# Optimization experiments

Hardware: AMD Instinct MI355X
Metric: run time of the kernel (lower is better)

The kernel has to match this reference:

```python
import jax, jax.numpy as jnp
import numpy as np

N = 16384
E = 524288
IN_DIM, H1, H2 = 256, 128, 64


def setup_inputs() -> dict:
    key = jax.random.key(0)
    ks = jax.random.split(key, 9)
    features = jax.random.normal(ks[0], (N, IN_DIM), dtype=jnp.float32)
    src = jax.random.randint(ks[1], (E,), 0, N, dtype=jnp.int32)
    dst = jax.random.randint(ks[2], (E,), 0, N, dtype=jnp.int32)
    s = 0.1
    W1 = jax.random.normal(ks[3], (IN_DIM, H1), dtype=jnp.float32) * s
    b1 = jnp.zeros((H1,), dtype=jnp.float32)
    W2 = jax.random.normal(ks[4], (H1, H1), dtype=jnp.float32) * s
    b2 = jnp.zeros((H1,), dtype=jnp.float32)
    W3 = jax.random.normal(ks[5], (H1, H2), dtype=jnp.float32) * s
    b3 = jnp.zeros((H2,), dtype=jnp.float32)
    return {"features": features, "src": src, "dst": dst,
            "W1": W1, "b1": b1, "W2": W2, "b2": b2, "W3": W3, "b3": b3}


def _degree_norms(src, dst):
    ones = jnp.ones(src.shape[0], dtype=jnp.float32)
    deg_out = jax.ops.segment_sum(ones, src, num_segments=N)
    deg_in = jax.ops.segment_sum(ones, dst, num_segments=N)
    # allow_zero_in_degree=True with norm='both': clamp degree to min 1
    norm_out = jax.lax.rsqrt(jnp.maximum(deg_out, 1.0))  # [N]
    norm_in = jax.lax.rsqrt(jnp.maximum(deg_in, 1.0))    # [N]
    return norm_out, norm_in


def _graph_conv(h, src, dst, norm_out, norm_in, W, b, relu):
    # DGL GraphConv, norm='both': D_in^{-1/2} A^T (D_out^{-1/2} h) W + b
    h = h * norm_out[:, None]
    msg = h[src]                                   # gather [E, d]
    agg = jax.ops.segment_sum(msg, dst, num_segments=N)  # scatter-add [N, d]
    out = agg * norm_in[:, None] @ W + b
    return jax.nn.relu(out) if relu else out


def reference(features, src, dst, W1, b1, W2, b2, W3, b3):
    norm_out, norm_in = _degree_norms(src, dst)
    h = _graph_conv(features, src, dst, norm_out, norm_in, W1, b1, True)
    h = _graph_conv(h, src, dst, norm_out, norm_in, W2, b2, True)
    z = _graph_conv(h, src, dst, norm_out, norm_in, W3, b3, False)  # [N, H2]
    adj_rec = jax.nn.sigmoid(z @ z.T)  # [N, N]
    return adj_rec, z
```

## Files before the change

### kernel.cpp

```cpp
#include <hip/hip_runtime.h>
#include <hip/hip_bf16.h>

#define NN 16384
#define EE 524288

constexpr int D0 = 256, D1 = 128, D2 = 64;

typedef __attribute__((ext_vector_type(8))) short short8;
typedef __attribute__((ext_vector_type(4))) float f32x4;

__device__ __forceinline__ float b2f(ushort u) {
  union { unsigned int i; float f; } x;
  x.i = ((unsigned int)u) << 16;
  return x.f;
}


__global__ __launch_bounds__(256) void count_deg_kernel(
    const int* __restrict__ src, const int* __restrict__ dst,
    int* __restrict__ deg_out, int* __restrict__ deg_in) {
  int e = blockIdx.x * 256 + threadIdx.x;
  if (e < EE) {
    atomicAdd(&deg_out[src[e]], 1);
    atomicAdd(&deg_in[dst[e]], 1);
  }
}

__global__ __launch_bounds__(256) void norm_kernel(
    const int* __restrict__ deg_out, const int* __restrict__ deg_in,
    float* __restrict__ norm_out, float* __restrict__ norm_in) {
  int i = blockIdx.x * 256 + threadIdx.x;
  if (i < NN) {
    norm_out[i] = rsqrtf(fmaxf((float)deg_out[i], 1.0f));
    norm_in[i]  = rsqrtf(fmaxf((float)deg_in[i], 1.0f));
  }
}

__global__ __launch_bounds__(256) void prefix_kernel(
    const int* __restrict__ deg_in, int* __restrict__ row_ptr,
    int* __restrict__ cursor) {
  __shared__ int part[256];
  int t = threadIdx.x;
  int base = t * 64;
  int s = 0;
  for (int j = 0; j < 64; ++j) s += deg_in[base + j];
  part[t] = s;
  __syncthreads();
  for (int off = 1; off < 256; off <<= 1) {
    int add = (t >= off) ? part[t - off] : 0;
    __syncthreads();
    part[t] += add;
    __syncthreads();
  }
  int run = (t == 0) ? 0 : part[t - 1];
  for (int j = 0; j < 64; ++j) {
    row_ptr[base + j] = run;
    cursor[base + j] = run;
    run += deg_in[base + j];
  }
  if (t == 255) row_ptr[NN] = run;
}

__global__ __launch_bounds__(256) void fill_csr_kernel(
    const int* __restrict__ src, const int* __restrict__ dst,
    int* __restrict__ cursor, int* __restrict__ csr_src) {
  int e = blockIdx.x * 256 + threadIdx.x;
  if (e < EE) {
    int pos = atomicAdd(&cursor[dst[e]], 1);
    csr_src[pos] = src[e];
  }
}


template<int DIN, int DOUT, bool OBF16>
__global__ __launch_bounds__(256) void gemm_kernel(
    const float* __restrict__ h, const float* __restrict__ W,
    const float* __restrict__ norm_out, float* __restrict__ tf,
    ushort* __restrict__ tb) {
  constexpr int W4 = DOUT / 4;
  constexpr int RG = 256 / W4;
  constexpr int RPT = 32 / RG;
  __shared__ float A[32][DIN];
  int tid = threadIdx.x;
  int r0 = blockIdx.x * 32;
  constexpr int NF4 = 32 * DIN / 4;
  for (int q = tid; q < NF4; q += 256) {
    int r = q / (DIN / 4);
    int c = q % (DIN / 4);
    float4 x = *(const float4*)&h[(size_t)(r0 + r) * DIN + c * 4];
    float no = norm_out[r0 + r];
    x.x *= no; x.y *= no; x.z *= no; x.w *= no;
    *(float4*)&A[r][c * 4] = x;
  }
  __syncthreads();
  int c4 = tid % W4;
  int rg = tid / W4;
  float4 acc[RPT];
#pragma unroll
  for (int j = 0; j < RPT; ++j) acc[j] = make_float4(0.f, 0.f, 0.f, 0.f);
  const float* Wp = W + c4 * 4;
#pragma unroll 2
  for (int k = 0; k < DIN; ++k) {
    float4 w = *(const float4*)&Wp[(size_t)k * DOUT];
#pragma unroll
    for (int j = 0; j < RPT; ++j) {
      float a = A[rg + j * RG][k];
      acc[j].x += a * w.x; acc[j].y += a * w.y;
      acc[j].z += a * w.z; acc[j].w += a * w.w;
    }
  }
#pragma unroll
  for (int j = 0; j < RPT; ++j) {
    size_t row = (size_t)(r0 + rg + j * RG);
    if (OBF16) {
      ushort4 o;
      __hip_bfloat16 h0 = __float2bfloat16(acc[j].x);
      __hip_bfloat16 h1 = __float2bfloat16(acc[j].y);
      __hip_bfloat16 h2 = __float2bfloat16(acc[j].z);
      __hip_bfloat16 h3 = __float2bfloat16(acc[j].w);
      o.x = *reinterpret_cast<ushort*>(&h0);
      o.y = *reinterpret_cast<ushort*>(&h1);
      o.z = *reinterpret_cast<ushort*>(&h2);
      o.w = *reinterpret_cast<ushort*>(&h3);
      *(ushort4*)&tb[row * DOUT + c4 * 4] = o;
    } else {
      *(float4*)&tf[row * DOUT + c4 * 4] = acc[j];
    }
  }
}


template<int DOUT, bool RELU>
__global__ __launch_bounds__(256) void gather_bf16_kernel(
    const ushort* __restrict__ t, const float* __restrict__ bias,
    const float* __restrict__ norm_in, const int* __restrict__ row_ptr,
    const int* __restrict__ csr, float* __restrict__ out) {
  constexpr int G8 = DOUT / 8;
  constexpr int S = 256 / G8;
  __shared__ float red[S][G8][8];
  int tid = threadIdx.x;
  int c8 = tid % G8, slot = tid / G8;
  int v = blockIdx.x;
  int k0 = row_ptr[v], k1 = row_ptr[v + 1];
  float a[8];
#pragma unroll
  for (int i = 0; i < 8; ++i) a[i] = 0.f;
  for (int k = k0 + slot; k < k1; k += S) {
    int s = csr[k];
    short8 m = *(const short8*)&t[(size_t)s * DOUT + c8 * 8];
#pragma unroll
    for (int i = 0; i < 8; ++i) a[i] += b2f((ushort)m[i]);
  }
#pragma unroll
  for (int i = 0; i < 8; ++i) red[slot][c8][i] = a[i];
  __syncthreads();
#pragma unroll
  for (int s = S / 2; s >= 1; s >>= 1) {
    if (slot < s) {
#pragma unroll
      for (int i = 0; i < 8; ++i) red[slot][c8][i] += red[slot + s][c8][i];
    }
    __syncthreads();
  }
  if (tid < G8) {
    float ni = norm_in[v];
    float o[8];
#pragma unroll
    for (int i = 0; i < 8; ++i) {
      o[i] = red[0][tid][i] * ni + bias[tid * 8 + i];
      if (RELU) o[i] = fmaxf(o[i], 0.f);
    }
    *(float4*)&out[(size_t)v * DOUT + tid * 8] = make_float4(o[0], o[1], o[2], o[3]);
    *(float4*)&out[(size_t)v * DOUT + tid * 8 + 4] = make_float4(o[4], o[5], o[6], o[7]);
  }
}


template<int DOUT, bool RELU>
__global__ __launch_bounds__(256) void gather_f32_kernel(
    const float* __restrict__ t, const float* __restrict__ bias,
    const float* __restrict__ norm_in, const int* __restrict__ row_ptr,
    const int* __restrict__ csr, float* __restrict__ out,
    ushort* __restrict__ zb) {
  constexpr int W4 = DOUT / 4;
  constexpr int S = 256 / W4;
  __shared__ float4 red[256];
  int tid = threadIdx.x;
  int c4 = tid % W4, slot = tid / W4;
  int v = blockIdx.x;
  int k0 = row_ptr[v], k1 = row_ptr[v + 1];
  float4 acc = make_float4(0.f, 0.f, 0.f, 0.f);
  for (int k = k0 + slot; k < k1; k += S) {
    int s = csr[k];
    float4 m = *(const float4*)&t[(size_t)s * DOUT + c4 * 4];
    acc.x += m.x; acc.y += m.y; acc.z += m.z; acc.w += m.w;
  }
  red[tid] = acc;
  __syncthreads();
  if (tid < W4) {
    float4 a = red[tid];
#pragma unroll
    for (int s = 1; s < S; ++s) {
      float4 b = red[s * W4 + tid];
      a.x += b.x; a.y += b.y; a.z += b.z; a.w += b.w;
    }
    float ni = norm_in[v];
    float4 b4 = *(const float4*)&bias[tid * 4];
    a.x = a.x * ni + b4.x; a.y = a.y * ni + b4.y;
    a.z = a.z * ni + b4.z; a.w = a.w * ni + b4.w;
    if (RELU) {
      a.x = fmaxf(a.x, 0.f); a.y = fmaxf(a.y, 0.f);
      a.z = fmaxf(a.z, 0.f); a.w = fmaxf(a.w, 0.f);
    }
    *(float4*)&out[(size_t)v * DOUT + tid * 4] = a;
    float vals[4] = {a.x, a.y, a.z, a.w};
    ushort4 ob;
    __hip_bfloat16 h0 = __float2bfloat16(vals[0]);
    __hip_bfloat16 h1 = __float2bfloat16(vals[1]);
    __hip_bfloat16 h2 = __float2bfloat16(vals[2]);
    __hip_bfloat16 h3 = __float2bfloat16(vals[3]);
    ob.x = *reinterpret_cast<ushort*>(&h0);
    ob.y = *reinterpret_cast<ushort*>(&h1);
    ob.z = *reinterpret_cast<ushort*>(&h2);
    ob.w = *reinterpret_cast<ushort*>(&h3);
    *(ushort4*)&zb[(size_t)v * DOUT + tid * 4] = ob;
  }
}


__global__ __launch_bounds__(256) void adj_mfma_kernel(
    const ushort* __restrict__ zb, float* __restrict__ C) {
  __shared__ ushort ZR[128 * 64];
  __shared__ ushort ZC[128 * 64];
  int t = threadIdx.x;
  int bx = blockIdx.x & 127, by = blockIdx.x >> 7;
  int row0 = by * 128, col0 = bx * 128;
  {
    int r = t >> 1;
    int ub = (t & 1) * 4;
    const float4* zr = (const float4*)(zb + (size_t)(row0 + r) * 64);
    const float4* zc = (const float4*)(zb + (size_t)(col0 + r) * 64);
    float4* LR = (float4*)ZR;
    float4* LC = (float4*)ZC;
#pragma unroll
    for (int u = 0; u < 4; ++u) {
      int sw = (ub + u) ^ (r & 7);
      LR[r * 8 + sw] = zr[ub + u];
      LC[r * 8 + sw] = zc[ub + u];
    }
  }
  __syncthreads();
  int l = t & 63, w = t >> 6;
  int wy = w >> 1, wx = w & 1;
  int lr = l & 15, lg = l >> 4;
  f32x4 acc[4][4];
#pragma unroll
  for (int i = 0; i < 4; ++i)
#pragma unroll
    for (int j = 0; j < 4; ++j) acc[i][j] = (f32x4){0.f, 0.f, 0.f, 0.f};

#pragma unroll
  for (int ks = 0; ks < 2; ++ks) {
    short8 af[4], bf_[4];
    int u = ks * 4 + lg;
#pragma unroll
    for (int i = 0; i < 4; ++i) {
      int ar = wy * 64 + i * 16 + lr;
      af[i] = *(const short8*)&ZR[ar * 64 + ((u ^ (ar & 7)) << 3)];
      int ac = wx * 64 + i * 16 + lr;
      bf_[i] = *(const short8*)&ZC[ac * 64 + ((u ^ (ac & 7)) << 3)];
    }
#pragma unroll
    for (int i = 0; i < 4; ++i)
#pragma unroll
      for (int j = 0; j < 4; ++j)
        acc[i][j] = __builtin_amdgcn_mfma_f32_16x16x32_bf16(
            bf_[j], af[i], acc[i][j], 0, 0, 0);
  }

#pragma unroll
  for (int i = 0; i < 4; ++i) {
    int crow = row0 + wy * 64 + i * 16 + lr;
    float* Crow = C + (size_t)crow * NN;
#pragma unroll
    for (int j = 0; j < 4; ++j) {
      int ccol = col0 + wx * 64 + j * 16 + lg * 4;
      float4 o;
      o.x = __builtin_amdgcn_rcpf(1.0f + __expf(-acc[i][j][0]));
      o.y = __builtin_amdgcn_rcpf(1.0f + __expf(-acc[i][j][1]));
      o.z = __builtin_amdgcn_rcpf(1.0f + __expf(-acc[i][j][2]));
      o.w = __builtin_amdgcn_rcpf(1.0f + __expf(-acc[i][j][3]));
      *(float4*)&Crow[ccol] = o;
    }
  }
}


extern "C" void kernel_launch(void* const* d_in, const int* in_sizes, int n_in,
                              void* d_out, int out_size, void* d_ws, size_t ws_size,
                              hipStream_t stream) {
  const float* features = (const float*)d_in[0];
  const int* src = (const int*)d_in[1];
  const int* dst = (const int*)d_in[2];
  const float* W1 = (const float*)d_in[3];
  const float* b1 = (const float*)d_in[4];
  const float* W2 = (const float*)d_in[5];
  const float* b2 = (const float*)d_in[6];
  const float* W3 = (const float*)d_in[7];
  const float* b3 = (const float*)d_in[8];

  float* outp = (float*)d_out;
  float* adj = outp;
  float* z = outp + (size_t)NN * NN;

  ushort* tb = (ushort*)adj;
  float* hbuf = adj + (size_t)NN * 64;
  float* t3 = adj + (size_t)NN * 192;

  float* wsf = (float*)d_ws;
  float* norm_out = wsf;
  float* norm_in = wsf + NN;
  int* deg_out = (int*)(wsf + 2 * NN);
  int* deg_in = deg_out + NN;
  int* row_ptr = deg_in + NN;
  int* cursor = row_ptr + NN + 256;
  int* csr_src = cursor + NN;
  ushort* zb = (ushort*)(csr_src + EE);

  hipMemsetAsync(deg_out, 0, 2 * NN * sizeof(int), stream);
  count_deg_kernel<<<EE / 256, 256, 0, stream>>>(src, dst, deg_out, deg_in);
  norm_kernel<<<NN / 256, 256, 0, stream>>>(deg_out, deg_in, norm_out, norm_in);
  prefix_kernel<<<1, 256, 0, stream>>>(deg_in, row_ptr, cursor);
  fill_csr_kernel<<<EE / 256, 256, 0, stream>>>(src, dst, cursor, csr_src);

  gemm_kernel<D0, D1, true><<<NN / 32, 256, 0, stream>>>(
      features, W1, norm_out, nullptr, tb);
  gather_bf16_kernel<D1, true><<<NN, 256, 0, stream>>>(
      tb, b1, norm_in, row_ptr, csr_src, hbuf);
  gemm_kernel<D1, D1, true><<<NN / 32, 256, 0, stream>>>(
      hbuf, W2, norm_out, nullptr, tb);
  gather_bf16_kernel<D1, true><<<NN, 256, 0, stream>>>(
      tb, b2, norm_in, row_ptr, csr_src, hbuf);
  gemm_kernel<D1, D2, false><<<NN / 32, 256, 0, stream>>>(
      hbuf, W3, norm_out, t3, nullptr);
  gather_f32_kernel<D2, false><<<NN, 256, 0, stream>>>(
      t3, b3, norm_in, row_ptr, csr_src, z, zb);

  adj_mfma_kernel<<<(NN / 128) * (NN / 128), 256, 0, stream>>>(zb, adj);
}
```

Before: 478.1 us.

## Use one wave per node for gathers, stage W in LDS, nontemporal adj stores

The aggregation kernels now assign one 64-lane wave per destination node, four nodes per block, and reduce across lanes with xor shuffles. This replaces the block-per-node layout whose LDS tree reduction and barriers left most threads idle at an average degree of about 32. The dense GEMM now stages W chunks in shared memory instead of reading them from global memory on every k step. The 1 GiB sigmoid adjacency output is written with nontemporal stores to avoid polluting the caches. These are several unrelated changes, and the extra LDS for W lowers the occupancy of the GEMM kernel.

```diff
diff --git a/kernel.cpp b/kernel.cpp
--- a/kernel.cpp
+++ b/kernel.cpp
@@ -13,6 +13,10 @@
   union { unsigned int i; float f; } x;
   x.i = ((unsigned int)u) << 16;
   return x.f;
+}
+__device__ __forceinline__ ushort f2b(float f) {
+  __hip_bfloat16 h = __float2bfloat16(f);
+  return *reinterpret_cast<ushort*>(&h);
 }
 
 
@@ -80,7 +84,9 @@
   constexpr int W4 = DOUT / 4;
   constexpr int RG = 256 / W4;
   constexpr int RPT = 32 / RG;
+  constexpr int KC = 64;
   __shared__ float A[32][DIN];
+  __shared__ float WC[KC][DOUT];
   int tid = threadIdx.x;
   int r0 = blockIdx.x * 32;
   constexpr int NF4 = 32 * DIN / 4;
@@ -92,21 +98,26 @@
     x.x *= no; x.y *= no; x.z *= no; x.w *= no;
     *(float4*)&A[r][c * 4] = x;
   }
-  __syncthreads();
   int c4 = tid % W4;
   int rg = tid / W4;
   float4 acc[RPT];
 #pragma unroll
   for (int j = 0; j < RPT; ++j) acc[j] = make_float4(0.f, 0.f, 0.f, 0.f);
-  const float* Wp = W + c4 * 4;
-#pragma unroll 2
-  for (int k = 0; k < DIN; ++k) {
-    float4 w = *(const float4*)&Wp[(size_t)k * DOUT];
-#pragma unroll
-    for (int j = 0; j < RPT; ++j) {
-      float a = A[rg + j * RG][k];
-      acc[j].x += a * w.x; acc[j].y += a * w.y;
-      acc[j].z += a * w.z; acc[j].w += a * w.w;
+
+  for (int kc = 0; kc < DIN / KC; ++kc) {
+    __syncthreads();
+    for (int q = tid; q < KC * W4; q += 256)
+      ((float4*)WC)[q] = ((const float4*)W)[(size_t)kc * KC * W4 + q];
+    __syncthreads();
+#pragma unroll 4
+    for (int k2 = 0; k2 < KC; ++k2) {
+      float4 w = *(const float4*)&WC[k2][c4 * 4];
+#pragma unroll
+      for (int j = 0; j < RPT; ++j) {
+        float a = A[rg + j * RG][kc * KC + k2];
+        acc[j].x += a * w.x; acc[j].y += a * w.y;
+        acc[j].z += a * w.z; acc[j].w += a * w.w;
+      }
     }
   }
 #pragma unroll
@@ -114,14 +125,8 @@
     size_t row = (size_t)(r0 + rg + j * RG);
     if (OBF16) {
       ushort4 o;
-      __hip_bfloat16 h0 = __float2bfloat16(acc[j].x);
-      __hip_bfloat16 h1 = __float2bfloat16(acc[j].y);
-      __hip_bfloat16 h2 = __float2bfloat16(acc[j].z);
-      __hip_bfloat16 h3 = __float2bfloat16(acc[j].w);
-      o.x = *reinterpret_cast<ushort*>(&h0);
-      o.y = *reinterpret_cast<ushort*>(&h1);
-      o.z = *reinterpret_cast<ushort*>(&h2);
-      o.w = *reinterpret_cast<ushort*>(&h3);
+      o.x = f2b(acc[j].x); o.y = f2b(acc[j].y);
+      o.z = f2b(acc[j].z); o.w = f2b(acc[j].w);
       *(ushort4*)&tb[row * DOUT + c4 * 4] = o;
     } else {
       *(float4*)&tf[row * DOUT + c4 * 4] = acc[j];
@@ -130,100 +135,61 @@
 }
 
 
-template<int DOUT, bool RELU>
-__global__ __launch_bounds__(256) void gather_bf16_kernel(
-    const ushort* __restrict__ t, const float* __restrict__ bias,
-    const float* __restrict__ norm_in, const int* __restrict__ row_ptr,
-    const int* __restrict__ csr, float* __restrict__ out) {
-  constexpr int G8 = DOUT / 8;
-  constexpr int S = 256 / G8;
-  __shared__ float red[S][G8][8];
-  int tid = threadIdx.x;
-  int c8 = tid % G8, slot = tid / G8;
-  int v = blockIdx.x;
-  int k0 = row_ptr[v], k1 = row_ptr[v + 1];
-  float a[8];
-#pragma unroll
-  for (int i = 0; i < 8; ++i) a[i] = 0.f;
-  for (int k = k0 + slot; k < k1; k += S) {
-    int s = csr[k];
-    short8 m = *(const short8*)&t[(size_t)s * DOUT + c8 * 8];
-#pragma unroll
-    for (int i = 0; i < 8; ++i) a[i] += b2f((ushort)m[i]);
-  }
-#pragma unroll
-  for (int i = 0; i < 8; ++i) red[slot][c8][i] = a[i];
-  __syncthreads();
-#pragma unroll
-  for (int s = S / 2; s >= 1; s >>= 1) {
-    if (slot < s) {
-#pragma unroll
-      for (int i = 0; i < 8; ++i) red[slot][c8][i] += red[slot + s][c8][i];
-    }
-    __syncthreads();
-  }
-  if (tid < G8) {
-    float ni = norm_in[v];
-    float o[8];
-#pragma unroll
-    for (int i = 0; i < 8; ++i) {
-      o[i] = red[0][tid][i] * ni + bias[tid * 8 + i];
-      if (RELU) o[i] = fmaxf(o[i], 0.f);
-    }
-    *(float4*)&out[(size_t)v * DOUT + tid * 8] = make_float4(o[0], o[1], o[2], o[3]);
-    *(float4*)&out[(size_t)v * DOUT + tid * 8 + 4] = make_float4(o[4], o[5], o[6], o[7]);
-  }
-}
-
-
-template<int DOUT, bool RELU>
-__global__ __launch_bounds__(256) void gather_f32_kernel(
-    const float* __restrict__ t, const float* __restrict__ bias,
+template<int DOUT, bool RELU, bool BF16IN, bool WRITEZB>
+__global__ __launch_bounds__(256) void gather_wave_kernel(
+    const void* __restrict__ tptr, const float* __restrict__ bias,
     const float* __restrict__ norm_in, const int* __restrict__ row_ptr,
     const int* __restrict__ csr, float* __restrict__ out,
     ushort* __restrict__ zb) {
-  constexpr int W4 = DOUT / 4;
-  constexpr int S = 256 / W4;
-  __shared__ float4 red[256];
-  int tid = threadIdx.x;
-  int c4 = tid % W4, slot = tid / W4;
-  int v = blockIdx.x;
+  constexpr int CH = DOUT / 8;
+  constexpr int SLOTS = 64 / CH;
+  int lane = threadIdx.x & 63;
+  int wid = threadIdx.x >> 6;
+  int v = blockIdx.x * 4 + wid;
+  int c8 = lane % CH;
+  int slot = lane / CH;
   int k0 = row_ptr[v], k1 = row_ptr[v + 1];
-  float4 acc = make_float4(0.f, 0.f, 0.f, 0.f);
-  for (int k = k0 + slot; k < k1; k += S) {
+  float a[8];
+#pragma unroll
+  for (int i = 0; i < 8; ++i) a[i] = 0.f;
+  for (int k = k0 + slot; k < k1; k += SLOTS) {
     int s = csr[k];
-    float4 m = *(const float4*)&t[(size_t)s * DOUT + c4 * 4];
-    acc.x += m.x; acc.y += m.y; acc.z += m.z; acc.w += m.w;
-  }
-  red[tid] = acc;
-  __syncthreads();
-  if (tid < W4) {
-    float4 a = red[tid];
-#pragma unroll
-    for (int s = 1; s < S; ++s) {
-      float4 b = red[s * W4 + tid];
-      a.x += b.x; a.y += b.y; a.z += b.z; a.w += b.w;
-    }
+    if (BF16IN) {
+      short8 m = *(const short8*)((const ushort*)tptr + (size_t)s * DOUT + c8 * 8);
+#pragma unroll
+      for (int i = 0; i < 8; ++i) a[i] += b2f((ushort)m[i]);
+    } else {
+      const float* tf = (const float*)tptr + (size_t)s * DOUT + c8 * 8;
+      float4 m0 = *(const float4*)tf;
+      float4 m1 = *(const float4*)(tf + 4);
+      a[0] += m0.x; a[1] += m0.y; a[2] += m0.z; a[3] += m0.w;
+      a[4] += m1.x; a[5] += m1.y; a[6] += m1.z; a[7] += m1.w;
+    }
+  }
+#pragma unroll
+  for (int m = CH; m < 64; m <<= 1) {
+#pragma unroll
+    for (int i = 0; i < 8; ++i) a[i] += __shfl_xor(a[i], m, 64);
+  }
+  if (slot == 0) {
     float ni = norm_in[v];
-    float4 b4 = *(const float4*)&bias[tid * 4];
-    a.x = a.x * ni + b4.x; a.y = a.y * ni + b4.y;
-    a.z = a.z * ni + b4.z; a.w = a.w * ni + b4.w;
-    if (RELU) {
-      a.x = fmaxf(a.x, 0.f); a.y = fmaxf(a.y, 0.f);
-      a.z = fmaxf(a.z, 0.f); a.w = fmaxf(a.w, 0.f);
-    }
-    *(float4*)&out[(size_t)v * DOUT + tid * 4] = a;
-    float vals[4] = {a.x, a.y, a.z, a.w};
-    ushort4 ob;
-    __hip_bfloat16 h0 = __float2bfloat16(vals[0]);
-    __hip_bfloat16 h1 = __float2bfloat16(vals[1]);
-    __hip_bfloat16 h2 = __float2bfloat16(vals[2]);
-    __hip_bfloat16 h3 = __float2bfloat16(vals[3]);
-    ob.x = *reinterpret_cast<ushort*>(&h0);
-    ob.y = *reinterpret_cast<ushort*>(&h1);
-    ob.z = *reinterpret_cast<ushort*>(&h2);
-    ob.w = *reinterpret_cast<ushort*>(&h3);
-    *(ushort4*)&zb[(size_t)v * DOUT + tid * 4] = ob;
+    float o[8];
+#pragma unroll
+    for (int i = 0; i < 8; ++i) {
+      o[i] = a[i] * ni + bias[c8 * 8 + i];
+      if (RELU) o[i] = fmaxf(o[i], 0.f);
+    }
+    float* op = out + (size_t)v * DOUT + c8 * 8;
+    *(float4*)op = make_float4(o[0], o[1], o[2], o[3]);
+    *(float4*)(op + 4) = make_float4(o[4], o[5], o[6], o[7]);
+    if (WRITEZB) {
+      ushort4 b0, b1;
+      b0.x = f2b(o[0]); b0.y = f2b(o[1]); b0.z = f2b(o[2]); b0.w = f2b(o[3]);
+      b1.x = f2b(o[4]); b1.y = f2b(o[5]); b1.z = f2b(o[6]); b1.w = f2b(o[7]);
+      ushort* zp = zb + (size_t)v * DOUT + c8 * 8;
+      *(ushort4*)zp = b0;
+      *(ushort4*)(zp + 4) = b1;
+    }
   }
 }
 
@@ -285,12 +251,12 @@
 #pragma unroll
     for (int j = 0; j < 4; ++j) {
       int ccol = col0 + wx * 64 + j * 16 + lg * 4;
-      float4 o;
-      o.x = __builtin_amdgcn_rcpf(1.0f + __expf(-acc[i][j][0]));
-      o.y = __builtin_amdgcn_rcpf(1.0f + __expf(-acc[i][j][1]));
-      o.z = __builtin_amdgcn_rcpf(1.0f + __expf(-acc[i][j][2]));
-      o.w = __builtin_amdgcn_rcpf(1.0f + __expf(-acc[i][j][3]));
-      *(float4*)&Crow[ccol] = o;
+      f32x4 o;
+      o[0] = __builtin_amdgcn_rcpf(1.0f + __expf(-acc[i][j][0]));
+      o[1] = __builtin_amdgcn_rcpf(1.0f + __expf(-acc[i][j][1]));
+      o[2] = __builtin_amdgcn_rcpf(1.0f + __expf(-acc[i][j][2]));
+      o[3] = __builtin_amdgcn_rcpf(1.0f + __expf(-acc[i][j][3]));
+      __builtin_nontemporal_store(o, (f32x4*)&Crow[ccol]);
     }
   }
 }
@@ -335,15 +301,15 @@
 
   gemm_kernel<D0, D1, true><<<NN / 32, 256, 0, stream>>>(
       features, W1, norm_out, nullptr, tb);
-  gather_bf16_kernel<D1, true><<<NN, 256, 0, stream>>>(
-      tb, b1, norm_in, row_ptr, csr_src, hbuf);
+  gather_wave_kernel<D1, true, true, false><<<NN / 4, 256, 0, stream>>>(
+      tb, b1, norm_in, row_ptr, csr_src, hbuf, nullptr);
   gemm_kernel<D1, D1, true><<<NN / 32, 256, 0, stream>>>(
       hbuf, W2, norm_out, nullptr, tb);
-  gather_bf16_kernel<D1, true><<<NN, 256, 0, stream>>>(
-      tb, b2, norm_in, row_ptr, csr_src, hbuf);
+  gather_wave_kernel<D1, true, true, false><<<NN / 4, 256, 0, stream>>>(
+      tb, b2, norm_in, row_ptr, csr_src, hbuf, nullptr);
   gemm_kernel<D1, D2, false><<<NN / 32, 256, 0, stream>>>(
       hbuf, W3, norm_out, t3, nullptr);
-  gather_f32_kernel<D2, false><<<NN, 256, 0, stream>>>(
+  gather_wave_kernel<D2, false, false, true><<<NN / 4, 256, 0, stream>>>(
       t3, b3, norm_in, row_ptr, csr_src, z, zb);
 
   adj_mfma_kernel<<<(NN / 128) * (NN / 128), 256, 0, stream>>>(zb, adj);
```

After: 512.1 us. 7.1% more time.
